# Kernel optimization log

Measured on AMD Instinct MI355X. Metric: run time of the kernel, lower is better.

## Reference

```python
import jax, jax.numpy as jnp
import numpy as np

B, G, N_IN, N_HID, N_OUT = 2, 4096, 8, 32, 32
ALPHA, BETA, BN_EPS = 0.005, 5e-5, 1e-5
EDGE_P = 0.05  # adjacency density


def _lin_init(k, fan_in, fan_out):
    k1, k2 = jax.random.split(k)
    lim = 1.0 / np.sqrt(fan_in)
    W = jax.random.uniform(k1, (fan_in, fan_out), minval=-lim, maxval=lim, dtype=jnp.float32)
    b = jax.random.uniform(k2, (fan_out,), minval=-lim, maxval=lim, dtype=jnp.float32)
    return W, b


def setup_inputs() -> dict:
    key = jax.random.key(0)
    ks = jax.random.split(key, 12)
    W_infer, b_infer = _lin_init(ks[0], N_IN, N_HID)
    W_e1, b_e1 = _lin_init(ks[1], 2 * N_HID, 1)
    W_e2, b_e2 = _lin_init(ks[2], 2 * N_HID, 1)
    W_n1, b_n1 = _lin_init(ks[3], 2 * N_HID, N_OUT)
    W_n2, b_n2 = _lin_init(ks[4], 2 * N_HID, N_OUT)
    W_m1, b_m1 = _lin_init(ks[5], 2 * N_HID, N_OUT)
    W_m2, b_m2 = _lin_init(ks[6], 2 * N_HID, N_OUT)
    x = jax.random.normal(ks[7], (B, G, N_IN), dtype=jnp.float32)
    edges1 = jax.random.bernoulli(ks[8], EDGE_P, (G, G)).astype(jnp.float32)
    edges2 = jax.random.bernoulli(ks[9], EDGE_P, (G, G)).astype(jnp.float32)
    bn_gamma = jnp.ones((G,), jnp.float32)
    bn_beta = jnp.zeros((G,), jnp.float32)
    return dict(x=x, edges1=edges1, edges2=edges2, W_infer=W_infer, b_infer=b_infer,
                W_e1=W_e1, b_e1=b_e1, W_e2=W_e2, b_e2=b_e2,
                W_n1=W_n1, b_n1=b_n1, W_n2=W_n2, b_n2=b_n2,
                W_m1=W_m1, b_m1=b_m1, W_m2=W_m2, b_m2=b_m2,
                bn_gamma=bn_gamma, bn_beta=bn_beta)


def _mp_block(x, adj, coef, W_e, b_e, W_n, b_n, W_m, b_m):
    # x: [B,G,H]. Torch builds edge feature at flat index k=i*G+j as cat([x_j, x_i])
    # (shape2 = col gather, shape1 = row gather). We keep the same math without
    # materializing the [B,G*G,2H] tensor.
    Hh = x.shape[-1]
    s_src = x @ W_e[:Hh]   # [B,G,1]  (x_j part of mlp_edge)
    s_dst = x @ W_e[Hh:]   # [B,G,1]  (x_i part of mlp_edge)
    logits = s_dst[:, :, None, 0] + s_src[:, None, :, 0] + b_e[0]   # [B,G,G] at (i,j)
    w = adj + coef * (adj == 0).astype(x.dtype)                     # ori_edge + coef*thres_edge
    e = jax.nn.sigmoid(logits) * w[None]                            # [B,G,G]
    # receive at node i: sum_j e_ij * [x_j, x_i]
    recv_src = jnp.einsum('bij,bjh->bih', e, x)                     # sum_j e_ij x_j
    recv_dst = x * jnp.sum(e, axis=2)[..., None]                    # x_i * sum_j e_ij
    recv = jnp.concatenate([recv_src, recv_dst], axis=-1)           # [B,G,2H]
    recv = jax.nn.elu(recv @ W_n + b_n)                             # nodes_mlp + elu
    upd = jnp.concatenate([recv, x], axis=-1) @ W_m + b_m           # mesg_merge (mode='cat')
    return jax.nn.elu(upd)


def _forward(x, edges1, edges2, W_infer, b_infer, W_e1, b_e1, W_e2, b_e2,
             W_n1, b_n1, W_n2, b_n2, W_m1, b_m1, W_m2, b_m2, bn_gamma, bn_beta):
    h = jax.nn.elu(x @ W_infer + b_infer)                           # infer + elu, [B,G,H]
    h = _mp_block(h, edges1, ALPHA, W_e1, b_e1, W_n1, b_n1, W_m1, b_m1)
    # BatchNorm1d(gene_num) on [B, G, n_out]: per-gene stats over (batch, feature)
    mu = jnp.mean(h, axis=(0, 2), keepdims=True)
    var = jnp.var(h, axis=(0, 2), keepdims=True)
    h = (h - mu) * jax.lax.rsqrt(var + BN_EPS)
    h = h * bn_gamma[None, :, None] + bn_beta[None, :, None]
    return _mp_block(h, edges2, BETA, W_e2, b_e2, W_n2, b_n2, W_m2, b_m2)


def reference(x, edges1, edges2, W_infer, b_infer, W_e1, b_e1, W_e2, b_e2,
              W_n1, b_n1, W_n2, b_n2, W_m1, b_m1, W_m2, b_m2, bn_gamma, bn_beta):
    return _forward(x, edges1, edges2, W_infer, b_infer, W_e1, b_e1, W_e2, b_e2,
                    W_n1, b_n1, W_n2, b_n2, W_m1, b_m1, W_m2, b_m2, bn_gamma, bn_beta)
```

## Files before the change

### kernel.cpp

```cpp
#include <hip/hip_runtime.h>

#define G 4096
#define BSZ 2
#define NIN 8
#define HID 32
#define NLOG2E (-1.4426950408889634f)

typedef __attribute__((ext_vector_type(8))) short short8;
typedef __attribute__((ext_vector_type(4))) float floatx4;
typedef unsigned short ushort_t;
typedef unsigned int uint_t;

__device__ __forceinline__ float elu1(float v) {
    return v > 0.f ? v : (__expf(v) - 1.f);
}
__device__ __forceinline__ ushort_t f2bf(float f) {
    unsigned u = __float_as_uint(f);
    u += 0x7fffu + ((u >> 16) & 1u);
    return (ushort_t)(u >> 16);
}

__global__ __launch_bounds__(256) void k_setup1(
    const float* __restrict__ x, const float* __restrict__ W,
    const float* __restrict__ bias, const float* __restrict__ We,
    float* __restrict__ h0, ushort_t* __restrict__ hTb,
    float* __restrict__ ssrc, float* __restrict__ sdst) {
    __shared__ __align__(16) ushort_t hs[HID][264];
    int tid = threadIdx.x;
    int t = blockIdx.x * 256 + tid;
    int b = t >> 12;
    int g0 = (blockIdx.x & 15) * 256;
    float xin[NIN];
    const float* xp = x + t * NIN;
#pragma unroll
    for (int k = 0; k < NIN; k++) xin[k] = xp[k];
    float ss = 0.f, sd = 0.f;
    float* hp = h0 + (size_t)t * HID;
#pragma unroll
    for (int o = 0; o < HID; o++) {
        float v = bias[o];
#pragma unroll
        for (int k = 0; k < NIN; k++) v += xin[k] * W[k * HID + o];
        v = elu1(v);
        hp[o] = v;
        hs[o][tid] = f2bf(v);
        ss += v * We[o];
        sd += v * We[HID + o];
    }
    ssrc[t] = ss;
    sdst[t] = sd;
    __syncthreads();
#pragma unroll
    for (int p = 0; p < 4; p++) {
        int row = p * 8 + (tid >> 5);
        int c = (tid & 31) * 8;
        short8 v8 = *(const short8*)&hs[row][c];
        *(short8*)(void*)&hTb[(size_t)(b * HID + row) * G + g0 + c] = v8;
    }
}

template <bool DO_BN>
__global__ __launch_bounds__(1024, 4) void k_fused(
    const float* __restrict__ adj, const float* __restrict__ ssrc,
    const float* __restrict__ sdst, const ushort_t* __restrict__ hTb_in,
    const float* __restrict__ bep, float coef, const float* __restrict__ hin,
    const float* __restrict__ Wn, const float* __restrict__ bnb,
    const float* __restrict__ Wm, const float* __restrict__ bmb,
    const float* __restrict__ gamma, const float* __restrict__ beta,
    const float* __restrict__ We2, float* __restrict__ outp,
    ushort_t* __restrict__ hTb_out, float* __restrict__ s2s,
    float* __restrict__ s2d) {
    union SMemU {
        float ssm[BSZ][G];
        struct {
            float rec[32][68];
            float rec2[32][68];
            float esg[16][2];
            ushort_t tb[BSZ][HID][16];
        } p;
    };
    __shared__ __align__(16) SMemU sm;
    __shared__ __align__(16) uint_t abits[128][16];
    __shared__ __align__(16) float red[14][64][9];
    __shared__ __align__(16) float Wns[2048];
    __shared__ __align__(16) float Wms[2048];

    int tid = threadIdx.x;
    int g0 = blockIdx.x * 16;
    int l = tid & 63, w = tid >> 6;
    int b = w >> 3, jq = w & 7;

    if (tid < 512) {
        ((float4*)Wns)[tid] = ((const float4*)Wn)[tid];
    } else {
        int t2 = tid - 512;
        ((float4*)Wms)[t2] = ((const float4*)Wm)[t2];
    }
#pragma unroll
    for (int r = 0; r < 2; r++) {
        int idx = r * 4096 + tid * 4;
        int bb = idx >> 12, j = idx & 4095;
        float4 s4 = *(const float4*)&ssrc[bb * G + j];
        s4.x *= NLOG2E; s4.y *= NLOG2E; s4.z *= NLOG2E; s4.w *= NLOG2E;
        *(float4*)&sm.ssm[bb][j] = s4;
    }
    {
        int jw = tid >> 3;
        bool st = (tid & 7) == 0;
        int sh = (tid & 7) * 4;
#pragma unroll
        for (int s = 0; s < 16; s++) {
            float4 v4 = *(const float4*)&adj[(size_t)(g0 + s) * G + tid * 4];
            uint_t nib = (uint_t)(v4.x != 0.f) | ((uint_t)(v4.y != 0.f) << 1) |
                         ((uint_t)(v4.z != 0.f) << 2) | ((uint_t)(v4.w != 0.f) << 3);
            uint_t wd = nib << sh;
            wd |= __shfl_xor(wd, 1);
            wd |= __shfl_xor(wd, 2);
            wd |= __shfl_xor(wd, 4);
            if (st) abits[jw][s] = wd;
        }
    }

    int m = l & 15, kg = l >> 4;
    float sd2 = (sdst[b * G + g0 + m] + bep[0]) * NLOG2E;
    float wm1 = 1.f - coef;
    int jstart = jq * 512;
    const ushort_t* hb0 = hTb_in + (size_t)(b * HID + m) * G + jstart + kg * 8;
    const ushort_t* hb1 = hb0 + (size_t)16 * G;
    floatx4 c0 = {0.f, 0.f, 0.f, 0.f}, c1 = {0.f, 0.f, 0.f, 0.f};
    float es = 0.f;
    short8 pb0[2], pb1[2];
#pragma unroll
    for (int d = 0; d < 2; d++) {
        pb0[d] = *(const short8*)(const void*)(hb0 + d * 32);
        pb1[d] = *(const short8*)(const void*)(hb1 + d * 32);
    }
    __syncthreads();
    const float* svp = &sm.ssm[b][jstart + kg * 8];
    const uint_t* abp = &abits[jq * 16][m];

#pragma unroll 4
    for (int jc = 0; jc < 16; jc++) {
        int cur = jc & 1;
        short8 bf0 = pb0[cur], bf1 = pb1[cur];
        if (jc + 2 < 16) {
            int o = (jc + 2) * 32;
            pb0[cur] = *(const short8*)(const void*)(hb0 + o);
            pb1[cur] = *(const short8*)(const void*)(hb1 + o);
        }
        uint_t bw = abp[jc * 16];
        float4 s0 = *(const float4*)&svp[jc * 32];
        float4 s1 = *(const float4*)&svp[jc * 32 + 4];
        float sv[8] = {s0.x, s0.y, s0.z, s0.w, s1.x, s1.y, s1.z, s1.w};
        short8 af;
#pragma unroll
        for (int t = 0; t < 8; t++) {
            float bitf = (float)((bw >> (kg * 8 + t)) & 1u);
            float wgt = __builtin_fmaf(bitf, wm1, coef);
            float ex = exp2f(sd2 + sv[t]);
            float e = __builtin_amdgcn_rcpf(1.f + ex) * wgt;
            es += e;
            af[t] = (short)f2bf(e);
        }
        c0 = __builtin_amdgcn_mfma_f32_16x16x32_bf16(af, bf0, c0, 0, 0, 0);
        c1 = __builtin_amdgcn_mfma_f32_16x16x32_bf16(af, bf1, c1, 0, 0, 0);
    }
    if (jq) {
        int widx = b * 7 + jq - 1;
#pragma unroll
        for (int r = 0; r < 4; r++) {
            red[widx][l][r] = c0[r];
            red[widx][l][4 + r] = c1[r];
        }
        red[widx][l][8] = es;
    }
    __syncthreads();
    if (!jq) {
#pragma unroll
        for (int q = 0; q < 7; q++) {
            int widx = b * 7 + q;
#pragma unroll
            for (int r = 0; r < 4; r++) {
                c0[r] += red[widx][l][r];
                c1[r] += red[widx][l][4 + r];
            }
            es += red[widx][l][8];
        }
        es += __shfl_xor(es, 16);
        es += __shfl_xor(es, 32);
#pragma unroll
        for (int r = 0; r < 4; r++) {
            int gene = (l >> 4) * 4 + r;
            sm.p.rec[gene * 2 + b][m] = c0[r];
            sm.p.rec[gene * 2 + b][16 + m] = c1[r];
        }
        if (l < 16) sm.p.esg[l][b] = es;
    }
    __syncthreads();

    int rl = tid >> 5, hh = tid & 31;
    int gene = rl >> 1, bb = rl & 1;
    float xv = hin[((size_t)(bb * G + g0 + gene)) * HID + hh];
    sm.p.rec[rl][32 + hh] = xv * sm.p.esg[gene][bb];
    __syncthreads();

    float v = bnb[hh];
#pragma unroll
    for (int k4 = 0; k4 < 16; k4++) {
        float4 r4 = *(const float4*)&sm.p.rec[rl][k4 * 4];
        v += r4.x * Wns[(k4 * 4 + 0) * HID + hh];
        v += r4.y * Wns[(k4 * 4 + 1) * HID + hh];
        v += r4.z * Wns[(k4 * 4 + 2) * HID + hh];
        v += r4.w * Wns[(k4 * 4 + 3) * HID + hh];
    }
    v = elu1(v);
    sm.p.rec2[rl][hh] = v;
    sm.p.rec2[rl][32 + hh] = xv;
    float u = bmb[hh];
#pragma unroll
    for (int k4 = 0; k4 < 16; k4++) {
        float4 r4 = *(const float4*)&sm.p.rec2[rl][k4 * 4];
        u += r4.x * Wms[(k4 * 4 + 0) * HID + hh];
        u += r4.y * Wms[(k4 * 4 + 1) * HID + hh];
        u += r4.z * Wms[(k4 * 4 + 2) * HID + hh];
        u += r4.w * Wms[(k4 * 4 + 3) * HID + hh];
    }
    float h1v = elu1(u);
    if (!DO_BN) {
        outp[((size_t)(bb * G + g0 + gene)) * HID + hh] = h1v;
    } else {
        float s = h1v, sq = h1v * h1v;
#pragma unroll
        for (int mm = 32; mm; mm >>= 1) {
            s += __shfl_xor(s, mm);
            sq += __shfl_xor(sq, mm);
        }
        float mu = s * (1.f / 64.f);
        float var = sq * (1.f / 64.f) - mu * mu;
        float rstd = rsqrtf(var + 1e-5f);
        float hn = (h1v - mu) * rstd * gamma[g0 + gene] + beta[g0 + gene];
        outp[((size_t)(bb * G + g0 + gene)) * HID + hh] = hn;
        sm.p.tb[bb][hh][gene] = f2bf(hn);
        float ps = hn * We2[hh], pd = hn * We2[HID + hh];
#pragma unroll
        for (int mm = 16; mm; mm >>= 1) {
            ps += __shfl_xor(ps, mm);
            pd += __shfl_xor(pd, mm);
        }
        if (hh == 0) {
            s2s[bb * G + g0 + gene] = ps;
            s2d[bb * G + g0 + gene] = pd;
        }
        __syncthreads();
        if (tid < 128) {
            int b2 = tid >> 6, c = (tid >> 1) & 31, half = tid & 1;
            short8 v8 = *(const short8*)&sm.p.tb[b2][c][half * 8];
            *(short8*)(void*)&hTb_out[(size_t)(b2 * HID + c) * G + g0 + half * 8] = v8;
        }
    }
}

extern "C" void kernel_launch(void* const* d_in, const int* in_sizes, int n_in,
                              void* d_out, int out_size, void* d_ws, size_t ws_size,
                              hipStream_t stream) {
    const float* x      = (const float*)d_in[0];
    const float* edges1 = (const float*)d_in[1];
    const float* edges2 = (const float*)d_in[2];
    const float* W_inf  = (const float*)d_in[3];
    const float* b_inf  = (const float*)d_in[4];
    const float* W_e1   = (const float*)d_in[5];
    const float* b_e1   = (const float*)d_in[6];
    const float* W_e2   = (const float*)d_in[7];
    const float* b_e2   = (const float*)d_in[8];
    const float* W_n1   = (const float*)d_in[9];
    const float* b_n1   = (const float*)d_in[10];
    const float* W_n2   = (const float*)d_in[11];
    const float* b_n2   = (const float*)d_in[12];
    const float* W_m1   = (const float*)d_in[13];
    const float* b_m1   = (const float*)d_in[14];
    const float* W_m2   = (const float*)d_in[15];
    const float* b_m2   = (const float*)d_in[16];
    const float* bn_g   = (const float*)d_in[17];
    const float* bn_b   = (const float*)d_in[18];
    float* out = (float*)d_out;

    float* ws = (float*)d_ws;
    float* h0   = ws;
    float* h1n  = ws + 262144;
    float* s1s  = ws + 524288;
    float* s1d  = ws + 532480;
    float* s2s  = ws + 540672;
    float* s2d  = ws + 548864;
    ushort_t* hTb  = (ushort_t*)(ws + 557056);
    ushort_t* hTb2 = (ushort_t*)(ws + 688128);

    const float ALPHA = 0.005f, BETA = 5e-5f;

    k_setup1<<<32, 256, 0, stream>>>(x, W_inf, b_inf, W_e1, h0, hTb, s1s, s1d);
    k_fused<true><<<G / 16, 1024, 0, stream>>>(
        edges1, s1s, s1d, hTb, b_e1, ALPHA, h0, W_n1, b_n1, W_m1, b_m1,
        bn_g, bn_b, W_e2, h1n, hTb2, s2s, s2d);
    k_fused<false><<<G / 16, 1024, 0, stream>>>(
        edges2, s2s, s2d, hTb2, b_e2, BETA, h1n, W_n2, b_n2, W_m2, b_m2,
        nullptr, nullptr, nullptr, out, nullptr, nullptr, nullptr);
}
```

Baseline: 239.8 us.

## Replace cross-wave LDS reduction buffer with shared-memory atomics and raise occupancy hint

```diff
diff --git a/kernel.cpp b/kernel.cpp
--- a/kernel.cpp
+++ b/kernel.cpp
@@ -60,7 +60,7 @@
 }
 
 template <bool DO_BN>
-__global__ __launch_bounds__(1024, 4) void k_fused(
+__global__ __launch_bounds__(1024, 8) void k_fused(
     const float* __restrict__ adj, const float* __restrict__ ssrc,
     const float* __restrict__ sdst, const ushort_t* __restrict__ hTb_in,
     const float* __restrict__ bep, float coef, const float* __restrict__ hin,
@@ -81,7 +81,6 @@
     };
     __shared__ __align__(16) SMemU sm;
     __shared__ __align__(16) uint_t abits[128][16];
-    __shared__ __align__(16) float red[14][64][9];
     __shared__ __align__(16) float Wns[2048];
     __shared__ __align__(16) float Wms[2048];
 
@@ -165,37 +164,24 @@
         c0 = __builtin_amdgcn_mfma_f32_16x16x32_bf16(af, bf0, c0, 0, 0, 0);
         c1 = __builtin_amdgcn_mfma_f32_16x16x32_bf16(af, bf1, c1, 0, 0, 0);
     }
-    if (jq) {
-        int widx = b * 7 + jq - 1;
-#pragma unroll
-        for (int r = 0; r < 4; r++) {
-            red[widx][l][r] = c0[r];
-            red[widx][l][4 + r] = c1[r];
-        }
-        red[widx][l][8] = es;
-    }
-    __syncthreads();
-    if (!jq) {
-#pragma unroll
-        for (int q = 0; q < 7; q++) {
-            int widx = b * 7 + q;
-#pragma unroll
-            for (int r = 0; r < 4; r++) {
-                c0[r] += red[widx][l][r];
-                c1[r] += red[widx][l][4 + r];
-            }
-            es += red[widx][l][8];
-        }
-        es += __shfl_xor(es, 16);
-        es += __shfl_xor(es, 32);
-#pragma unroll
-        for (int r = 0; r < 4; r++) {
-            int gene = (l >> 4) * 4 + r;
-            sm.p.rec[gene * 2 + b][m] = c0[r];
-            sm.p.rec[gene * 2 + b][16 + m] = c1[r];
-        }
-        if (l < 16) sm.p.esg[l][b] = es;
-    }
+    __syncthreads();
+    {
+        float* rz = &sm.p.rec[0][0];
+        rz[tid] = 0.f;
+        rz[tid + 1024] = 0.f;
+        if (tid < 128) rz[tid + 2048] = 0.f;
+        if (tid < 32) ((float*)sm.p.esg)[tid] = 0.f;
+    }
+    __syncthreads();
+    es += __shfl_xor(es, 16);
+    es += __shfl_xor(es, 32);
+#pragma unroll
+    for (int r = 0; r < 4; r++) {
+        int gene = kg * 4 + r;
+        atomicAdd(&sm.p.rec[gene * 2 + b][m], c0[r]);
+        atomicAdd(&sm.p.rec[gene * 2 + b][16 + m], c1[r]);
+    }
+    if (l < 16) atomicAdd(&sm.p.esg[l][b], es);
     __syncthreads();
 
     int rl = tid >> 5, hh = tid & 31;
```

New measurement: 344.1 us. 1.44x slower.
